# Optimization experiments

Measured on AMD Instinct MI355X. Metric: run time of the kernel, lower is better.

The kernel has to match this reference:

```python
import jax, jax.numpy as jnp
import numpy as np

HID, NHEAD, NLAYERS = 128, 8, 6
BS, H, W = 1, 64, 128
HD = HID // NHEAD  # head dim = 16


def layer_norm(x, g, b, eps=1e-5):
    m = jnp.mean(x, -1, keepdims=True)
    v = jnp.mean((x - m) ** 2, -1, keepdims=True)
    return (x - m) * jax.lax.rsqrt(v + eps) * g + b


def mha_relative(query, kv, in_w, in_b, out_w, out_b, pos_enc, pos_idx, attn_mask, is_self):
    # query/kv: [W, N, C]; in_w: [3C, C]; pos_enc: [2W-1, C]; pos_idx: [W*W]
    w, n, c = query.shape
    if is_self:
        q, k, v = jnp.split(query @ in_w.T + in_b, 3, axis=-1)
    else:
        q = query @ in_w[:c].T + in_b[:c]
        k, v = jnp.split(kv @ in_w[c:].T + in_b[c:], 2, axis=-1)
    # relative positional bias: gather [2W-1,C] -> [W,W,C], project with q/k weights
    pos_sel = pos_enc[pos_idx].reshape(w, w, c)
    q_r, k_r = jnp.split(pos_sel @ in_w[:2 * c].T + in_b[:2 * c], 2, axis=-1)
    scale = HD ** -0.5
    q = (q * scale).reshape(w, n, NHEAD, HD)
    k = k.reshape(w, n, NHEAD, HD)
    v = v.reshape(w, n, NHEAD, HD)
    q_r = (q_r * scale).reshape(w, w, NHEAD, HD)
    k_r = k_r.reshape(w, w, NHEAD, HD)
    attn = (jnp.einsum('wnec,vnec->newv', q, k)
            + jnp.einsum('wnec,wvec->newv', q, k_r)
            + jnp.einsum('vnec,wvec->newv', k, q_r))  # [N,E,W,W]
    if attn_mask is not None:
        attn = attn + attn_mask[None, None]
    raw_attn = attn.sum(axis=1)  # [N,W,W] head-summed raw scores
    a = jax.nn.softmax(attn, axis=-1)
    v_o = jnp.einsum('newv,vnec->wnec', a, v).reshape(w, n, c)
    return v_o @ out_w.T + out_b, raw_attn


def setup_inputs() -> dict:
    key = jax.random.key(0)
    ks = jax.random.split(key, 8)
    f32 = jnp.float32
    s = 0.02
    d = {}
    d['feat_left'] = jax.random.normal(ks[0], (BS, HID, H, W), f32)
    d['feat_right'] = jax.random.normal(ks[1], (BS, HID, H, W), f32)
    d['pos_enc'] = jax.random.normal(ks[2], (2 * W - 1, HID), f32)
    d['self_ln_g'] = jnp.ones((NLAYERS, HID), f32)
    d['self_ln_b'] = jnp.zeros((NLAYERS, HID), f32)
    d['self_in_w'] = jax.random.normal(ks[3], (NLAYERS, 3 * HID, HID), f32) * s
    d['self_in_b'] = jnp.zeros((NLAYERS, 3 * HID), f32)
    d['self_out_w'] = jax.random.normal(ks[4], (NLAYERS, HID, HID), f32) * s
    d['self_out_b'] = jnp.zeros((NLAYERS, HID), f32)
    d['cross_ln1_g'] = jnp.ones((NLAYERS, HID), f32)
    d['cross_ln1_b'] = jnp.zeros((NLAYERS, HID), f32)
    d['cross_ln2_g'] = jnp.ones((NLAYERS, HID), f32)
    d['cross_ln2_b'] = jnp.zeros((NLAYERS, HID), f32)
    d['cross_in_w'] = jax.random.normal(ks[5], (NLAYERS, 3 * HID, HID), f32) * s
    d['cross_in_b'] = jnp.zeros((NLAYERS, 3 * HID), f32)
    d['cross_out_w'] = jax.random.normal(ks[6], (NLAYERS, HID, HID), f32) * s
    d['cross_out_b'] = jnp.zeros((NLAYERS, HID), f32)
    return d


def reference(feat_left, feat_right, pos_enc, self_ln_g, self_ln_b, self_in_w, self_in_b,
              self_out_w, self_out_b, cross_ln1_g, cross_ln1_b, cross_ln2_g, cross_ln2_b,
              cross_in_w, cross_in_b, cross_out_w, cross_out_b):
    bs, c, hn, w = feat_left.shape  # bs must be 1 (as in source)
    # [N,C,H,W] -> [W, H*N, C]
    fl = jnp.transpose(feat_left, (3, 2, 0, 1)).reshape(w, hn * bs, c)
    fr = jnp.transpose(feat_right, (3, 2, 0, 1)).reshape(w, hn * bs, c)
    HN = hn * bs
    # pos_indexes[i,j] = (w-1-i) + j, values in [0, 2w-2]
    pos_idx = ((w - 1 - jnp.arange(w))[:, None] + jnp.arange(w)[None, :]).reshape(-1)
    causal = jnp.triu(jnp.full((w, w), -jnp.inf, feat_left.dtype), k=1)
    feat = jnp.concatenate([fl, fr], axis=1)  # [W, 2HN, C]
    raw_attn = None
    for i in range(NLAYERS):
        # self attention over concatenated left+right rows
        f2 = layer_norm(feat, self_ln_g[i], self_ln_b[i])
        upd, _ = mha_relative(f2, f2, self_in_w[i], self_in_b[i], self_out_w[i],
                              self_out_b[i], pos_enc, pos_idx, None, True)
        feat = feat + upd
        left, right = feat[:, :HN], feat[:, HN:]
        # cross attention: left queries attend to norm2(right)
        # (source computes a right-update with norm1/flipped pos but discards it)
        l2 = layer_norm(left, cross_ln1_g[i], cross_ln1_b[i])
        r2 = layer_norm(right, cross_ln2_g[i], cross_ln2_b[i])
        mask = causal if i == NLAYERS - 1 else None
        upd, raw_attn = mha_relative(l2, r2, cross_in_w[i], cross_in_b[i], cross_out_w[i],
                                     cross_out_b[i], pos_enc, pos_idx, mask, False)
        left = left + upd
        feat = jnp.concatenate([left, right], axis=1)
    # [HN,W,W] -> [bs, hn, W, W]
    return jnp.transpose(raw_attn.reshape(hn, bs, w, w), (1, 0, 2, 3))
```

## Files before the change

kernel.cpp:

```cpp
#include <hip/hip_runtime.h>
#include <cmath>

#define CDIM 128

typedef __attribute__((ext_vector_type(8))) short bf16x8;
typedef __attribute__((ext_vector_type(4))) float f32x4;
typedef unsigned short u16;

__device__ inline unsigned pk2(float a, float b) {
    unsigned ua = __float_as_uint(a) + 0x8000u;
    unsigned ub = __float_as_uint(b) + 0x8000u;
    return (ua >> 16) | (ub & 0xffff0000u);
}
__device__ inline u16 pk1(float x) {
    return (u16)((__float_as_uint(x) + 0x8000u) >> 16);
}
__device__ inline float ubf(u16 u) { return __uint_as_float(((unsigned)u) << 16); }
__device__ inline float ulo(unsigned u) { return __uint_as_float(u << 16); }
__device__ inline float uhi(unsigned u) { return __uint_as_float(u & 0xffff0000u); }

__global__ __launch_bounds__(256) void setup1_kernel(const float* __restrict__ w0,
                                                     const float* __restrict__ w1,
                                                     const float* __restrict__ w2,
                                                     const float* __restrict__ w3,
                                                     const float* __restrict__ b0,
                                                     const float* __restrict__ b1,
                                                     u16* __restrict__ wout,
                                                     float* __restrict__ bout,
                                                     const float* __restrict__ FL,
                                                     const float* __restrict__ FR,
                                                     u16* __restrict__ feat) {
    __shared__ float t[32][33];
    int bb = blockIdx.x;
    if (bb < 786) {
        int idx = bb * 256 + threadIdx.x;
        if (idx < 196608) {
            const float* src; long off4; u16* dst;
            if (idx < 73728)       { src = w0; off4 = idx;           dst = wout; }
            else if (idx < 147456) { src = w1; off4 = idx - 73728;   dst = wout + 294912; }
            else if (idx < 172032) { src = w2; off4 = idx - 147456;  dst = wout + 589824; }
            else                   { src = w3; off4 = idx - 172032;  dst = wout + 688128; }
            float4 f = *(const float4*)(src + off4 * 4);
            *(uint2*)(dst + off4 * 4) = make_uint2(pk2(f.x, f.y), pk2(f.z, f.w));
        } else {
            int tt = idx - 196608;
            if (tt < 4608) bout[tt] = (tt < 2304) ? b0[tt] : b1[tt - 2304];
        }
        return;
    }
    int b = bb - 786;
    int cb = b & 3, wb = (b >> 2) & 3, n = b >> 4;
    const float* src = (n < 64) ? FL : FR;
    int nn = n & 63;
    int j = threadIdx.x & 31, i0 = threadIdx.x >> 5;
    #pragma unroll
    for (int p = 0; p < 4; p++) {
        int i = i0 + p * 8;
        t[i][j] = src[(cb * 32 + i) * 8192 + nn * 128 + wb * 32 + j];
    }
    __syncthreads();
    #pragma unroll
    for (int p = 0; p < 4; p++) {
        int i = i0 + p * 8;
        feat[((long)(wb * 32 + i) * 128 + n) * 128 + cb * 32 + j] = pk1(t[j][i]);
    }
}

__global__ __launch_bounds__(256, 4) void setup2_kernel(const u16* __restrict__ feat,
                                                        const float* __restrict__ g,
                                                        const float* __restrict__ b,
                                                        u16* __restrict__ lnB,
                                                        const float* __restrict__ Apos,
                                                        const u16* __restrict__ Wpp,
                                                        const float* __restrict__ biaspp,
                                                        u16* __restrict__ Cpp,
                                                        float scale) {
    __shared__ __align__(16) u16 sA[64 * 136];
    __shared__ __align__(16) u16 sW[64 * 136];
    int bb = blockIdx.x;
    int tid = threadIdx.x;
    if (bb < 1024) {
        int wv = tid >> 6, lane = tid & 63;
        float g0 = g[lane * 2], b0 = b[lane * 2];
        float g1 = g[lane * 2 + 1], b1 = b[lane * 2 + 1];
        #pragma unroll
        for (int rr = 0; rr < 4; rr++) {
            long m = (long)bb * 16 + wv * 4 + rr;
            unsigned u = *(const unsigned*)(feat + m * 128 + lane * 2);
            float x0 = ulo(u), x1 = uhi(u);
            float s = x0 + x1, q = x0 * x0 + x1 * x1;
            #pragma unroll
            for (int off = 1; off < 64; off <<= 1) {
                s += __shfl_xor(s, off);
                q += __shfl_xor(q, off);
            }
            float mean = s * (1.f / 128.f);
            float var = q * (1.f / 128.f) - mean * mean;
            float rs = rsqrtf(var + 1e-5f);
            float y0 = (x0 - mean) * rs * g0 + b0;
            float y1 = (x1 - mean) * rs * g1 + b1;
            *(unsigned*)(lnB + m * 128 + lane * 2) = pk2(y0, y1);
        }
        return;
    }
    int b2 = bb - 1024;
    int bx = b2 & 3, byy = (b2 >> 2) & 3, z = b2 >> 4;
    const int M = 255, N = 256;
    const u16* W = Wpp + (long)z * 49152;
    const float* bias = biaspp + z * 384;
    u16* C = Cpp + (long)z * 65280;
    int row0 = byy * 64, col0 = bx * 64;
    float4 zf4 = make_float4(0.f, 0.f, 0.f, 0.f);
    int kc = tid & 31;
    #pragma unroll
    for (int i = 0; i < 8; i++) {
        int r = (tid + i * 256) >> 5;
        int m = row0 + r;
        int jn = col0 + r;
        float4 fa = (m < M) ? *(const float4*)(Apos + (long)m * 128 + kc * 4) : zf4;
        uint2 uw = make_uint2(0u, 0u);
        if (jn < N) uw = *(const uint2*)(W + (long)jn * 128 + kc * 4);
        *(uint2*)&sA[r * 136 + kc * 4] = make_uint2(pk2(fa.x, fa.y), pk2(fa.z, fa.w));
        *(uint2*)&sW[r * 136 + kc * 4] = uw;
    }
    __syncthreads();

    int wv = tid >> 6, lane = tid & 63, quad = lane >> 4, col = lane & 15;
    f32x4 z4 = {0.f, 0.f, 0.f, 0.f};
    f32x4 acc0 = z4, acc1 = z4, acc2 = z4, acc3 = z4;
    #pragma unroll
    for (int kb = 0; kb < 4; kb++) {
        bf16x8 a = *(const bf16x8*)&sA[(wv * 16 + col) * 136 + kb * 32 + quad * 8];
        bf16x8 b0 = *(const bf16x8*)&sW[(0 * 16 + col) * 136 + kb * 32 + quad * 8];
        bf16x8 b1 = *(const bf16x8*)&sW[(1 * 16 + col) * 136 + kb * 32 + quad * 8];
        bf16x8 b2 = *(const bf16x8*)&sW[(2 * 16 + col) * 136 + kb * 32 + quad * 8];
        bf16x8 b3 = *(const bf16x8*)&sW[(3 * 16 + col) * 136 + kb * 32 + quad * 8];
        acc0 = __builtin_amdgcn_mfma_f32_16x16x32_bf16(a, b0, acc0, 0, 0, 0);
        acc1 = __builtin_amdgcn_mfma_f32_16x16x32_bf16(a, b1, acc1, 0, 0, 0);
        acc2 = __builtin_amdgcn_mfma_f32_16x16x32_bf16(a, b2, acc2, 0, 0, 0);
        acc3 = __builtin_amdgcn_mfma_f32_16x16x32_bf16(a, b3, acc3, 0, 0, 0);
    }
    int mrow = row0 + wv * 16 + quad * 4;
    #pragma unroll
    for (int tc = 0; tc < 4; tc++) {
        f32x4 acc = tc == 0 ? acc0 : tc == 1 ? acc1 : tc == 2 ? acc2 : acc3;
        int jn = col0 + tc * 16 + col;
        if (jn >= N) continue;
        float bs = bias[jn];
        float sc = (jn < 128) ? scale : 1.f;
        long db = ((long)(jn >> 4) * 255) * 16 + (jn & 15);
        #pragma unroll
        for (int reg = 0; reg < 4; reg++) {
            int m = mrow + reg;
            if (m >= M) continue;
            C[db + (long)m * 16] = pk1((acc[reg] + bs) * sc);
        }
    }
}

__global__ __launch_bounds__(256, 3) void gemm_qkv128_kernel(const u16* __restrict__ A,
                                                             const u16* __restrict__ W,
                                                             const float* __restrict__ bias,
                                                             u16* __restrict__ C,
                                                             float scale) {
    __shared__ __align__(16) u16 sA[128 * 136];
    __shared__ __align__(16) u16 sW[64 * 136];
    int tid = threadIdx.x;
    int row0 = blockIdx.y * 128, col0 = blockIdx.x * 64;
    int kc = tid & 31;
    #pragma unroll
    for (int i = 0; i < 16; i++) {
        int r = (tid + i * 256) >> 5;
        *(uint2*)&sA[r * 136 + kc * 4] =
            *(const uint2*)(A + (long)(row0 + r) * 128 + kc * 4);
    }
    #pragma unroll
    for (int i = 0; i < 8; i++) {
        int r = (tid + i * 256) >> 5;
        *(uint2*)&sW[r * 136 + kc * 4] =
            *(const uint2*)(W + (long)(col0 + r) * 128 + kc * 4);
    }
    __syncthreads();

    int wv = tid >> 6, lane = tid & 63, quad = lane >> 4, col = lane & 15;
    f32x4 z4 = {0.f, 0.f, 0.f, 0.f};
    f32x4 accA0 = z4, accA1 = z4, accA2 = z4, accA3 = z4;
    f32x4 accB0 = z4, accB1 = z4, accB2 = z4, accB3 = z4;
    #pragma unroll
    for (int kb = 0; kb < 4; kb++) {
        bf16x8 a0 = *(const bf16x8*)&sA[(wv * 32 + col) * 136 + kb * 32 + quad * 8];
        bf16x8 a1 = *(const bf16x8*)&sA[(wv * 32 + 16 + col) * 136 + kb * 32 + quad * 8];
        bf16x8 b0 = *(const bf16x8*)&sW[(0 * 16 + col) * 136 + kb * 32 + quad * 8];
        bf16x8 b1 = *(const bf16x8*)&sW[(1 * 16 + col) * 136 + kb * 32 + quad * 8];
        bf16x8 b2 = *(const bf16x8*)&sW[(2 * 16 + col) * 136 + kb * 32 + quad * 8];
        bf16x8 b3 = *(const bf16x8*)&sW[(3 * 16 + col) * 136 + kb * 32 + quad * 8];
        accA0 = __builtin_amdgcn_mfma_f32_16x16x32_bf16(a0, b0, accA0, 0, 0, 0);
        accA1 = __builtin_amdgcn_mfma_f32_16x16x32_bf16(a0, b1, accA1, 0, 0, 0);
        accA2 = __builtin_amdgcn_mfma_f32_16x16x32_bf16(a0, b2, accA2, 0, 0, 0);
        accA3 = __builtin_amdgcn_mfma_f32_16x16x32_bf16(a0, b3, accA3, 0, 0, 0);
        accB0 = __builtin_amdgcn_mfma_f32_16x16x32_bf16(a1, b0, accB0, 0, 0, 0);
        accB1 = __builtin_amdgcn_mfma_f32_16x16x32_bf16(a1, b1, accB1, 0, 0, 0);
        accB2 = __builtin_amdgcn_mfma_f32_16x16x32_bf16(a1, b2, accB2, 0, 0, 0);
        accB3 = __builtin_amdgcn_mfma_f32_16x16x32_bf16(a1, b3, accB3, 0, 0, 0);
    }
    long woff = (long)blockIdx.y * 16;
    #pragma unroll
    for (int st = 0; st < 2; st++) {
        int nrow = wv * 32 + st * 16 + quad * 4;
        #pragma unroll
        for (int tc = 0; tc < 4; tc++) {
            f32x4 acc;
            if (st == 0) acc = tc == 0 ? accA0 : tc == 1 ? accA1 : tc == 2 ? accA2 : accA3;
            else         acc = tc == 0 ? accB0 : tc == 1 ? accB1 : tc == 2 ? accB2 : accB3;
            int jn = col0 + tc * 16 + col;
            float bs = bias[jn];
            float sc = (jn < 128) ? scale : 1.f;
            long db = ((long)(jn >> 4) * 128) * 2048 + woff + (jn & 15);
            #pragma unroll
            for (int reg = 0; reg < 4; reg++)
                C[db + (long)(nrow + reg) * 2048] = pk1((acc[reg] + bs) * sc);
        }
    }
}

__global__ __launch_bounds__(256, 2) void f1_out_self_cqkv_kernel(
        const u16* __restrict__ A,
        const u16* __restrict__ W,
        const float* __restrict__ bias,
        u16* __restrict__ feat,
        const float* __restrict__ g1, const float* __restrict__ b1,
        const float* __restrict__ g2, const float* __restrict__ b2,
        const float* __restrict__ sng, const float* __restrict__ snb,
        u16* __restrict__ lnB,
        const u16* __restrict__ Wcr,
        const float* __restrict__ biac,
        u16* __restrict__ QKV,
        float scale) {
    __shared__ __align__(16) u16 sA[64 * 136];
    __shared__ __align__(16) u16 sW[128 * 136];
    int tid = threadIdx.x;
    int by = blockIdx.x;
    int row0 = by * 64;
    int right = by & 1;
    int w = by >> 1;
    int kc = tid & 31;
    uint2 pw[16];
    #pragma unroll
    for (int i = 0; i < 8; i++) {
        int r = (tid + i * 256) >> 5;
        *(uint2*)&sA[r * 136 + kc * 4] = *(const uint2*)(A + (long)(row0 + r) * 128 + kc * 4);
    }
    #pragma unroll
    for (int i = 0; i < 16; i++) {
        int r = (tid + i * 256) >> 5;
        *(uint2*)&sW[r * 136 + kc * 4] = *(const uint2*)(W + (long)r * 128 + kc * 4);
    }
    {
        int w0 = right ? 128 : 0;
        #pragma unroll
        for (int i = 0; i < 16; i++) {
            int r = (tid + i * 256) >> 5;
            pw[i] = *(const uint2*)(Wcr + (long)(w0 + r) * 128 + kc * 4);
        }
    }
    __syncthreads();

    int wv = tid >> 6, lane = tid & 63, quad = lane >> 4, col = lane & 15;
    f32x4 acc[8] = {};
    #pragma unroll
    for (int kb = 0; kb < 4; kb++) {
        bf16x8 a = *(const bf16x8*)&sA[(wv * 16 + col) * 136 + kb * 32 + quad * 8];
        #pragma unroll
        for (int tc = 0; tc < 8; tc++) {
            bf16x8 b = *(const bf16x8*)&sW[(tc * 16 + col) * 136 + kb * 32 + quad * 8];
            acc[tc] = __builtin_amdgcn_mfma_f32_16x16x32_bf16(a, b, acc[tc], 0, 0, 0);
        }
    }
    __syncthreads();

    #pragma unroll
    for (int i = 0; i < 16; i++) {
        int r = (tid + i * 256) >> 5;
        *(uint2*)&sW[r * 136 + kc * 4] = pw[i];
    }
    if (right) {
        #pragma unroll
        for (int i = 0; i < 16; i++) {
            int r = (tid + i * 256) >> 5;
            pw[i] = *(const uint2*)(Wcr + (long)(256 + r) * 128 + kc * 4);
        }
    }

    const float* gA = right ? g2 : g1;
    const float* bA = right ? b2 : b1;
    float gAv[8], bAv[8], gBv[8], bBv[8], bsv[8];
    bool doB = (sng != nullptr) && right;
    #pragma unroll
    for (int tc = 0; tc < 8; tc++) {
        int jn = tc * 16 + col;
        gAv[tc] = gA[jn]; bAv[tc] = bA[jn]; bsv[tc] = bias[jn];
        if (doB) { gBv[tc] = sng[jn]; bBv[tc] = snb[jn]; }
    }
    #pragma unroll
    for (int reg = 0; reg < 4; reg++) {
        int nloc = wv * 16 + quad * 4 + reg;
        long m = row0 + nloc;
        long rb = m * 128;
        float o[8];
        float s = 0.f, q = 0.f;
        #pragma unroll
        for (int tc = 0; tc < 8; tc++) {
            int jn = tc * 16 + col;
            float v = acc[tc][reg] + bsv[tc] + ubf(feat[rb + jn]);
            o[tc] = v; s += v; q += v * v;
        }
        #pragma unroll
        for (int off = 1; off < 16; off <<= 1) {
            s += __shfl_xor(s, off);
            q += __shfl_xor(q, off);
        }
        float mean = s * (1.f / 128.f);
        float var = q * (1.f / 128.f) - mean * mean;
        float rs = rsqrtf(var + 1e-5f);
        #pragma unroll
        for (int tc = 0; tc < 8; tc++) {
            int jn = tc * 16 + col;
            feat[rb + jn] = pk1(o[tc]);
            float ln = (o[tc] - mean) * rs;
            sA[nloc * 136 + jn] = pk1(ln * gAv[tc] + bAv[tc]);
            if (doB) lnB[rb + jn] = pk1(ln * gBv[tc] + bBv[tc]);
        }
    }
    __syncthreads();

    int passes = right ? 2 : 1;
    #pragma unroll
    for (int p = 0; p < 2; p++) {
        if (p >= passes) break;
        if (p) {
            __syncthreads();
            #pragma unroll
            for (int i = 0; i < 16; i++) {
                int r = (tid + i * 256) >> 5;
                *(uint2*)&sW[r * 136 + kc * 4] = pw[i];
            }
            __syncthreads();
        }
        int wrow0 = right ? (128 + p * 128) : 0;
        f32x4 acb[8] = {};
        #pragma unroll
        for (int kb = 0; kb < 4; kb++) {
            bf16x8 a = *(const bf16x8*)&sA[(wv * 16 + col) * 136 + kb * 32 + quad * 8];
            #pragma unroll
            for (int tc = 0; tc < 8; tc++) {
                bf16x8 b = *(const bf16x8*)&sW[(tc * 16 + col) * 136 + kb * 32 + quad * 8];
                acb[tc] = __builtin_amdgcn_mfma_f32_16x16x32_bf16(a, b, acb[tc], 0, 0, 0);
            }
        }
        float sc = right ? 1.f : scale;
        int nrow = wv * 16 + quad * 4;
        #pragma unroll
        for (int tc = 0; tc < 8; tc++) {
            int jn = tc * 16 + col;
            float bs = biac[wrow0 + jn];
            int strip = right ? (8 + p * 8 + (jn >> 4)) : (jn >> 4);
            long db = (long)strip * 131072 + w * 16 + (jn & 15);
            #pragma unroll
            for (int reg = 0; reg < 4; reg++)
                QKV[db + (long)(nrow + reg) * 2048] = pk1((acb[tc][reg] + bs) * sc);
        }
    }
}

__global__ __launch_bounds__(256, 2) void f2_out_cross_qkv_kernel(
        const u16* __restrict__ A,
        const u16* __restrict__ W,
        const float* __restrict__ bias,
        u16* __restrict__ feat,
        const float* __restrict__ sng,
        const float* __restrict__ snb,
        const u16* __restrict__ lnBg,
        const u16* __restrict__ Wsl,
        const float* __restrict__ biasq,
        u16* __restrict__ QKV,
        float scale) {
    __shared__ __align__(16) u16 sA[64 * 136];
    __shared__ __align__(16) u16 sW[128 * 136];
    int tid = threadIdx.x;
    int t = blockIdx.x;
    int right = t & 1, w = t >> 1;
    int kc = tid & 31;
    uint2 pw[16];
    if (!right) {
        #pragma unroll
        for (int i = 0; i < 8; i++) {
            int r = (tid + i * 256) >> 5;
            *(uint2*)&sA[r * 136 + kc * 4] =
                *(const uint2*)(A + (long)(w * 64 + r) * 128 + kc * 4);
        }
        #pragma unroll
        for (int i = 0; i < 16; i++) {
            int r = (tid + i * 256) >> 5;
            *(uint2*)&sW[r * 136 + kc * 4] = *(const uint2*)(W + (long)r * 128 + kc * 4);
        }
    } else {
        #pragma unroll
        for (int i = 0; i < 8; i++) {
            int r = (tid + i * 256) >> 5;
            *(uint2*)&sA[r * 136 + kc * 4] =
                *(const uint2*)(lnBg + (long)(w * 128 + 64 + r) * 128 + kc * 4);
        }
    }
    #pragma unroll
    for (int i = 0; i < 16; i++) {
        int r = (tid + i * 256) >> 5;
        pw[i] = *(const uint2*)(Wsl + (long)r * 128 + kc * 4);
    }
    __syncthreads();

    int wv = tid >> 6, lane = tid & 63, quad = lane >> 4, col = lane & 15;
    if (!right) {
        f32x4 acc[8] = {};
        #pragma unroll
        for (int kb = 0; kb < 4; kb++) {
            bf16x8 a = *(const bf16x8*)&sA[(wv * 16 + col) * 136 + kb * 32 + quad * 8];
            #pragma unroll
            for (int tc = 0; tc < 8; tc++) {
                bf16x8 b = *(const bf16x8*)&sW[(tc * 16 + col) * 136 + kb * 32 + quad * 8];
                acc[tc] = __builtin_amdgcn_mfma_f32_16x16x32_bf16(a, b, acc[tc], 0, 0, 0);
            }
        }
        __syncthreads();
        float gBv[8], bBv[8], bsv[8];
        #pragma unroll
        for (int tc = 0; tc < 8; tc++) {
            int jn = tc * 16 + col;
            gBv[tc] = sng[jn]; bBv[tc] = snb[jn]; bsv[tc] = bias[jn];
        }
        #pragma unroll
        for (int reg = 0; reg < 4; reg++) {
            int nloc = wv * 16 + quad * 4 + reg;
            long rb = ((long)w * 128 + nloc) * 128;
            float o[8];
            float s = 0.f, q = 0.f;
            #pragma unroll
            for (int tc = 0; tc < 8; tc++) {
                int jn = tc * 16 + col;
                float v = acc[tc][reg] + bsv[tc] + ubf(feat[rb + jn]);
                o[tc] = v; s += v; q += v * v;
            }
            #pragma unroll
            for (int off = 1; off < 16; off <<= 1) {
                s += __shfl_xor(s, off);
                q += __shfl_xor(q, off);
            }
            float mean = s * (1.f / 128.f);
            float var = q * (1.f / 128.f) - mean * mean;
            float rs = rsqrtf(var + 1e-5f);
            #pragma unroll
            for (int tc = 0; tc < 8; tc++) {
                int jn = tc * 16 + col;
                feat[rb + jn] = pk1(o[tc]);
                sA[nloc * 136 + jn] = pk1((o[tc] - mean) * rs * gBv[tc] + bBv[tc]);
            }
        }
    }
    #pragma unroll
    for (int i = 0; i < 16; i++) {
        int r = (tid + i * 256) >> 5;
        *(uint2*)&sW[r * 136 + kc * 4] = pw[i];
    }
    #pragma unroll
    for (int i = 0; i < 16; i++) {
        int r = (tid + i * 256) >> 5;
        pw[i] = *(const uint2*)(Wsl + (long)(128 + r) * 128 + kc * 4);
    }
    __syncthreads();

    int n0 = right ? 64 : 0;
    #pragma unroll
    for (int p = 0; p < 3; p++) {
        if (p) {
            __syncthreads();
            #pragma unroll
            for (int i = 0; i < 16; i++) {
                int r = (tid + i * 256) >> 5;
                *(uint2*)&sW[r * 136 + kc * 4] = pw[i];
            }
            if (p < 2) {
                #pragma unroll
                for (int i = 0; i < 16; i++) {
                    int r = (tid + i * 256) >> 5;
                    pw[i] = *(const uint2*)(Wsl + (long)(256 + r) * 128 + kc * 4);
                }
            }
            __syncthreads();
        }
        f32x4 ac[8] = {};
        #pragma unroll
        for (int kb = 0; kb < 4; kb++) {
            bf16x8 a = *(const bf16x8*)&sA[(wv * 16 + col) * 136 + kb * 32 + quad * 8];
            #pragma unroll
            for (int tc = 0; tc < 8; tc++) {
                bf16x8 b = *(const bf16x8*)&sW[(tc * 16 + col) * 136 + kb * 32 + quad * 8];
                ac[tc] = __builtin_amdgcn_mfma_f32_16x16x32_bf16(a, b, ac[tc], 0, 0, 0);
            }
        }
        int nrow = n0 + wv * 16 + quad * 4;
        #pragma unroll
        for (int tc = 0; tc < 8; tc++) {
            int jn = p * 128 + tc * 16 + col;
            float bs = biasq[jn];
            float sc = (jn < 128) ? scale : 1.f;
            long db = (long)(jn >> 4) * 262144 + w * 16 + (jn & 15);
            #pragma unroll
            for (int reg = 0; reg < 4; reg++)
                QKV[db + (long)(nrow + reg) * 2048] = pk1((ac[tc][reg] + bs) * sc);
        }
    }
}

__global__ __launch_bounds__(512, 8) void attn_kernel(const u16* __restrict__ QKV,
                                                      const u16* __restrict__ PPL,
                                                      u16* __restrict__ VO,
                                                      float* __restrict__ RAW,
                                                      int NN, int causal) {
    __shared__ __align__(16) u16 sm[19584];
    const int SKV = 0, SA = 2176;
    int e = blockIdx.x, n = blockIdx.y;
    int tid = threadIdx.x;
    int wv = tid >> 6, lane = tid & 63, quad = lane >> 4, col = lane & 15;

    const u16* qb = QKV + ((long)e * NN + n) * 2048;
    const u16* kb = QKV + ((long)(8 + e) * NN + n) * 2048;
    const u16* vb = QKV + ((long)(16 + e) * NN + n) * 2048;
    const u16* qr = PPL + (long)e * 4080;
    const u16* kr = PPL + (long)(8 + e) * 4080;

    bf16x8 zf = {0, 0, 0, 0, 0, 0, 0, 0};
    f32x4 z4 = {0.f, 0.f, 0.f, 0.f};
    bf16x8 aQ = zf, aK = zf;
    if (quad < 2) {
        aQ = *(const bf16x8*)(qb + (wv * 16 + col) * 16 + quad * 8);
        aK = *(const bf16x8*)(kb + (wv * 16 + col) * 16 + quad * 8);
    }
    {
        int row = tid >> 2, c = tid & 3;
        *(uint2*)&sm[SKV + row * 16 + c * 4] = *(const uint2*)(kb + row * 16 + c * 4);
    }
    __syncthreads();

    f32x4 s1[8];
    #pragma unroll
    for (int tv = 0; tv < 8; tv++) {
        bf16x8 b = zf;
        if (quad < 2) b = *(const bf16x8*)&sm[SKV + (tv * 16 + col) * 16 + quad * 8];
        s1[tv] = __builtin_amdgcn_mfma_f32_16x16x32_bf16(aQ, b, z4, 0, 0, 0);
    }
    int wbq = wv * 16 + quad * 4;
    int s2lo = 7 - wv;
    #pragma unroll 3
    for (int tt = 0; tt < 9; tt++) {
        int tr = s2lo + tt;
        bf16x8 b = zf;
        if (quad < 2) b = *(const bf16x8*)(kr + (tr * 16 + col) * 16 + quad * 8);
        f32x4 d = __builtin_amdgcn_mfma_f32_16x16x32_bf16(aQ, b, z4, 0, 0, 0);
        #pragma unroll
        for (int reg = 0; reg < 4; reg++) {
            int v = tr * 16 + col - 127 + wbq + reg;
            if (v >= 0 && v < 128) sm[SA + (wbq + reg) * 136 + v] = pk1(d[reg]);
        }
    }
    __syncthreads();
    {
        int row = tid >> 2, c = tid & 3;
        uint2 uv = *(const uint2*)(vb + row * 16 + c * 4);
        sm[SKV + (c * 4 + 0) * 136 + row] = (u16)(uv.x & 0xffffu);
        sm[SKV + (c * 4 + 1) * 136 + row] = (u16)(uv.x >> 16);
        sm[SKV + (c * 4 + 2) * 136 + row] = (u16)(uv.y & 0xffffu);
        sm[SKV + (c * 4 + 3) * 136 + row] = (u16)(uv.y >> 16);
    }
    #pragma unroll 3
    for (int tt = 0; tt < 9; tt++) {
        int tr = wv + tt;
        bf16x8 b = zf;
        if (quad < 2) b = *(const bf16x8*)(qr + (tr * 16 + col) * 16 + quad * 8);
        f32x4 d = __builtin_amdgcn_mfma_f32_16x16x32_bf16(aK, b, z4, 0, 0, 0);
        #pragma unroll
        for (int reg = 0; reg < 4; reg++) {
            int v = wbq + reg;
            int w = 127 + v - (tr * 16 + col);
            if (w >= 0 && w < 128) {
                int addr = SA + w * 136 + v;
                sm[addr] = pk1(ubf(sm[addr]) + d[reg]);
            }
        }
    }
    __syncthreads();

    float rs0 = 0.f, rs1 = 0.f, rs2 = 0.f, rs3 = 0.f;
    #pragma unroll
    for (int tv = 0; tv < 8; tv++) {
        f32x4 c = s1[tv];
        int v = tv * 16 + col;
        #pragma unroll
        for (int reg = 0; reg < 4; reg++) {
            int w = wbq + reg;
            int addr = SA + w * 136 + v;
            float a = c[reg] + ubf(sm[addr]);
            bool live = !(causal && v > w);
            float p = live ? __expf(a) : 0.f;
            if (RAW) RAW[(long)n * 16384 + w * 128 + v] = live ? a : 0.f;
            sm[addr] = pk1(p);
            if (reg == 0) rs0 += p; else if (reg == 1) rs1 += p;
            else if (reg == 2) rs2 += p; else rs3 += p;
        }
    }
    #pragma unroll
    for (int o = 1; o < 16; o <<= 1) {
        rs0 += __shfl_xor(rs0, o);
        rs1 += __shfl_xor(rs1, o);
        rs2 += __shfl_xor(rs2, o);
        rs3 += __shfl_xor(rs3, o);
    }
    __syncthreads();

    f32x4 o4 = z4;
    #pragma unroll
    for (int kb = 0; kb < 4; kb++) {
        bf16x8 a = *(const bf16x8*)&sm[SA + (wv * 16 + col) * 136 + kb * 32 + quad * 8];
        bf16x8 b = *(const bf16x8*)&sm[SKV + col * 136 + kb * 32 + quad * 8];
        o4 = __builtin_amdgcn_mfma_f32_16x16x32_bf16(a, b, o4, 0, 0, 0);
    }
    float iv0 = 1.f / rs0, iv1 = 1.f / rs1, iv2 = 1.f / rs2, iv3 = 1.f / rs3;
    VO[(long)((wbq + 0) * NN + n) * CDIM + e * 16 + col] = pk1(o4[0] * iv0);
    VO[(long)((wbq + 1) * NN + n) * CDIM + e * 16 + col] = pk1(o4[1] * iv1);
    VO[(long)((wbq + 2) * NN + n) * CDIM + e * 16 + col] = pk1(o4[2] * iv2);
    VO[(long)((wbq + 3) * NN + n) * CDIM + e * 16 + col] = pk1(o4[3] * iv3);
}

extern "C" void kernel_launch(void* const* d_in, const int* in_sizes, int n_in,
                              void* d_out, int out_size, void* d_ws, size_t ws_size,
                              hipStream_t stream) {
    const float* FL         = (const float*)d_in[0];
    const float* FR         = (const float*)d_in[1];
    const float* pos_enc    = (const float*)d_in[2];
    const float* self_ln_g  = (const float*)d_in[3];
    const float* self_ln_b  = (const float*)d_in[4];
    const float* self_in_w  = (const float*)d_in[5];
    const float* self_in_b  = (const float*)d_in[6];
    const float* self_out_w = (const float*)d_in[7];
    const float* self_out_b = (const float*)d_in[8];
    const float* cr_ln1_g   = (const float*)d_in[9];
    const float* cr_ln1_b   = (const float*)d_in[10];
    const float* cr_ln2_g   = (const float*)d_in[11];
    const float* cr_ln2_b   = (const float*)d_in[12];
    const float* cr_in_w    = (const float*)d_in[13];
    const float* cr_in_b    = (const float*)d_in[14];
    const float* cr_out_w   = (const float*)d_in[15];
    const float* cr_out_b   = (const float*)d_in[16];

    float* ws       = (float*)d_ws;
    u16*   feat     = (u16*)ws;
    u16*   vo       = (u16*)(ws + 1048576);
    u16*   qkvS     = (u16*)(ws + 2097152);
    u16*   pp_self  = (u16*)(ws + 5242880);
    u16*   pp_cross = pp_self + 391680;
    u16*   wbf      = (u16*)(ws + 5634560);
    u16*   wsel_in  = wbf;
    u16*   wcr_in   = wbf + 294912;
    u16*   wsel_out = wbf + 589824;
    u16*   wcr_out  = wbf + 688128;
    float* bin      = ws + 6027776;
    u16*   lnB      = (u16*)(ws + 7080960);
    float* out      = (float*)d_out;

    const float scale = 0.25f;

    setup1_kernel<<<2834, 256, 0, stream>>>(self_in_w, cr_in_w, self_out_w, cr_out_w,
                                            self_in_b, cr_in_b, wbf, bin,
                                            FL, FR, feat);
    setup2_kernel<<<1216, 256, 0, stream>>>(feat, self_ln_g, self_ln_b, lnB,
                                            pos_enc, wsel_in, bin, pp_self, scale);
    gemm_qkv128_kernel<<<dim3(6, 128), 256, 0, stream>>>(lnB, wsel_in,
                                                         self_in_b, qkvS, scale);

    for (int i = 0; i < 6; i++) {
        int last = (i == 5);
        attn_kernel<<<dim3(8, 128), 512, 0, stream>>>(qkvS, pp_self + i * 65280,
                                                      vo, nullptr, 128, 0);
        f1_out_self_cqkv_kernel<<<256, 256, 0, stream>>>(vo, wsel_out + i * 16384,
                                                         self_out_b + i * 128, feat,
                                                         cr_ln1_g + i * 128, cr_ln1_b + i * 128,
                                                         cr_ln2_g + i * 128, cr_ln2_b + i * 128,
                                                         last ? nullptr : self_ln_g + (i + 1) * 128,
                                                         last ? nullptr : self_ln_b + (i + 1) * 128,
                                                         lnB,
                                                         wcr_in + i * 49152,
                                                         cr_in_b + i * 384,
                                                         qkvS, scale);

        attn_kernel<<<dim3(8, 64), 512, 0, stream>>>(qkvS, pp_cross + i * 65280,
                                                     vo, last ? out : nullptr,
                                                     64, last);
        if (!last) {
            f2_out_cross_qkv_kernel<<<256, 256, 0, stream>>>(vo, wcr_out + i * 16384,
                                                             cr_out_b + i * 128, feat,
                                                             self_ln_g + (i + 1) * 128,
                                                             self_ln_b + (i + 1) * 128,
                                                             lnB,
                                                             wsel_in + (i + 1) * 49152,
                                                             self_in_b + (i + 1) * 384,
                                                             qkvS, scale);
        }
    }
}
```

Measured before the change: 480.9 us.

## Warp-specialize fused out-proj/QKV kernels with 512 threads and weight prefetch

```diff
diff --git a/kernel.cpp b/kernel.cpp
--- a/kernel.cpp
+++ b/kernel.cpp
@@ -223,7 +223,7 @@
     }
 }
 
-__global__ __launch_bounds__(256, 2) void f1_out_self_cqkv_kernel(
+__global__ __launch_bounds__(512, 1) void f1_out_self_cqkv_kernel(
         const u16* __restrict__ A,
         const u16* __restrict__ W,
         const float* __restrict__ bias,
@@ -243,136 +243,168 @@
     int row0 = by * 64;
     int right = by & 1;
     int w = by >> 1;
-    int kc = tid & 31;
-    uint2 pw[16];
-    #pragma unroll
-    for (int i = 0; i < 8; i++) {
-        int r = (tid + i * 256) >> 5;
-        *(uint2*)&sA[r * 136 + kc * 4] = *(const uint2*)(A + (long)(row0 + r) * 128 + kc * 4);
-    }
-    #pragma unroll
-    for (int i = 0; i < 16; i++) {
-        int r = (tid + i * 256) >> 5;
-        *(uint2*)&sW[r * 136 + kc * 4] = *(const uint2*)(W + (long)r * 128 + kc * 4);
-    }
-    {
+    int wv = tid >> 6, lane = tid & 63, quad = lane >> 4, col = lane & 15;
+    int koff = quad * 8;
+    int t2 = tid & 255;
+    int kc = t2 & 31;
+    uint2 pw0[16], pw1[16];
+
+    if (tid < 256) {
+        #pragma unroll
+        for (int i = 0; i < 8; i++) {
+            int r = (t2 + i * 256) >> 5;
+            *(uint2*)&sA[r * 136 + kc * 4] = *(const uint2*)(A + (long)(row0 + r) * 128 + kc * 4);
+        }
+        #pragma unroll
+        for (int i = 0; i < 16; i++) {
+            int r = (t2 + i * 256) >> 5;
+            *(uint2*)&sW[r * 136 + kc * 4] = *(const uint2*)(W + (long)r * 128 + kc * 4);
+        }
+    } else {
         int w0 = right ? 128 : 0;
         #pragma unroll
         for (int i = 0; i < 16; i++) {
-            int r = (tid + i * 256) >> 5;
-            pw[i] = *(const uint2*)(Wcr + (long)(w0 + r) * 128 + kc * 4);
-        }
-    }
-    __syncthreads();
-
-    int wv = tid >> 6, lane = tid & 63, quad = lane >> 4, col = lane & 15;
+            int r = (t2 + i * 256) >> 5;
+            pw0[i] = *(const uint2*)(Wcr + (long)(w0 + r) * 128 + kc * 4);
+        }
+        if (right) {
+            #pragma unroll
+            for (int i = 0; i < 16; i++) {
+                int r = (t2 + i * 256) >> 5;
+                pw1[i] = *(const uint2*)(Wcr + (long)(256 + r) * 128 + kc * 4);
+            }
+        }
+    }
+    __syncthreads();
+
     f32x4 acc[8] = {};
-    #pragma unroll
-    for (int kb = 0; kb < 4; kb++) {
-        bf16x8 a = *(const bf16x8*)&sA[(wv * 16 + col) * 136 + kb * 32 + quad * 8];
-        #pragma unroll
-        for (int tc = 0; tc < 8; tc++) {
-            bf16x8 b = *(const bf16x8*)&sW[(tc * 16 + col) * 136 + kb * 32 + quad * 8];
-            acc[tc] = __builtin_amdgcn_mfma_f32_16x16x32_bf16(a, b, acc[tc], 0, 0, 0);
-        }
-    }
-    __syncthreads();
-
-    #pragma unroll
-    for (int i = 0; i < 16; i++) {
-        int r = (tid + i * 256) >> 5;
-        *(uint2*)&sW[r * 136 + kc * 4] = pw[i];
-    }
-    if (right) {
-        #pragma unroll
-        for (int i = 0; i < 16; i++) {
-            int r = (tid + i * 256) >> 5;
-            pw[i] = *(const uint2*)(Wcr + (long)(256 + r) * 128 + kc * 4);
-        }
-    }
-
-    const float* gA = right ? g2 : g1;
-    const float* bA = right ? b2 : b1;
-    float gAv[8], bAv[8], gBv[8], bBv[8], bsv[8];
-    bool doB = (sng != nullptr) && right;
-    #pragma unroll
-    for (int tc = 0; tc < 8; tc++) {
-        int jn = tc * 16 + col;
-        gAv[tc] = gA[jn]; bAv[tc] = bA[jn]; bsv[tc] = bias[jn];
-        if (doB) { gBv[tc] = sng[jn]; bBv[tc] = snb[jn]; }
-    }
-    #pragma unroll
-    for (int reg = 0; reg < 4; reg++) {
-        int nloc = wv * 16 + quad * 4 + reg;
-        long m = row0 + nloc;
-        long rb = m * 128;
-        float o[8];
-        float s = 0.f, q = 0.f;
+    if (tid < 256) {
+        #pragma unroll
+        for (int kb = 0; kb < 4; kb++) {
+            bf16x8 a = *(const bf16x8*)&sA[(wv * 16 + col) * 136 + kb * 32 + koff];
+            #pragma unroll
+            for (int tc = 0; tc < 8; tc++) {
+                bf16x8 b = *(const bf16x8*)&sW[(tc * 16 + col) * 136 + kb * 32 + koff];
+                acc[tc] = __builtin_amdgcn_mfma_f32_16x16x32_bf16(a, b, acc[tc], 0, 0, 0);
+            }
+        }
+    }
+    __syncthreads();
+
+    if (tid < 256) {
+        const float* gA = right ? g2 : g1;
+        const float* bA = right ? b2 : b1;
+        float gAv[8], bAv[8], gBv[8], bBv[8], bsv[8];
+        bool doB = (sng != nullptr) && right;
         #pragma unroll
         for (int tc = 0; tc < 8; tc++) {
             int jn = tc * 16 + col;
-            float v = acc[tc][reg] + bsv[tc] + ubf(feat[rb + jn]);
-            o[tc] = v; s += v; q += v * v;
-        }
-        #pragma unroll
-        for (int off = 1; off < 16; off <<= 1) {
-            s += __shfl_xor(s, off);
-            q += __shfl_xor(q, off);
-        }
-        float mean = s * (1.f / 128.f);
-        float var = q * (1.f / 128.f) - mean * mean;
-        float rs = rsqrtf(var + 1e-5f);
-        #pragma unroll
-        for (int tc = 0; tc < 8; tc++) {
-            int jn = tc * 16 + col;
-            feat[rb + jn] = pk1(o[tc]);
-            float ln = (o[tc] - mean) * rs;
-            sA[nloc * 136 + jn] = pk1(ln * gAv[tc] + bAv[tc]);
-            if (doB) lnB[rb + jn] = pk1(ln * gBv[tc] + bBv[tc]);
-        }
-    }
-    __syncthreads();
-
-    int passes = right ? 2 : 1;
-    #pragma unroll
-    for (int p = 0; p < 2; p++) {
-        if (p >= passes) break;
-        if (p) {
-            __syncthreads();
-            #pragma unroll
-            for (int i = 0; i < 16; i++) {
-                int r = (tid + i * 256) >> 5;
-                *(uint2*)&sW[r * 136 + kc * 4] = pw[i];
-            }
-            __syncthreads();
-        }
-        int wrow0 = right ? (128 + p * 128) : 0;
-        f32x4 acb[8] = {};
+            gAv[tc] = gA[jn]; bAv[tc] = bA[jn]; bsv[tc] = bias[jn];
+            if (doB) { gBv[tc] = sng[jn]; bBv[tc] = snb[jn]; }
+        }
+        #pragma unroll
+        for (int reg = 0; reg < 4; reg++) {
+            int nloc = wv * 16 + quad * 4 + reg;
+            long m = row0 + nloc;
+            long rb = m * 128;
+            float o[8];
+            float s = 0.f, q = 0.f;
+            #pragma unroll
+            for (int tc = 0; tc < 8; tc++) {
+                int jn = tc * 16 + col;
+                float v = acc[tc][reg] + bsv[tc] + ubf(feat[rb + jn]);
+                o[tc] = v; s += v; q += v * v;
+            }
+            #pragma unroll
+            for (int off = 1; off < 16; off <<= 1) {
+                s += __shfl_xor(s, off);
+                q += __shfl_xor(q, off);
+            }
+            float mean = s * (1.f / 128.f);
+            float var = q * (1.f / 128.f) - mean * mean;
+            float rs = rsqrtf(var + 1e-5f);
+            #pragma unroll
+            for (int tc = 0; tc < 8; tc++) {
+                int jn = tc * 16 + col;
+                feat[rb + jn] = pk1(o[tc]);
+                float ln = (o[tc] - mean) * rs;
+                sA[nloc * 136 + jn] = pk1(ln * gAv[tc] + bAv[tc]);
+                if (doB) lnB[rb + jn] = pk1(ln * gBv[tc] + bBv[tc]);
+            }
+        }
+    } else {
+        #pragma unroll
+        for (int i = 0; i < 16; i++) {
+            int r = (t2 + i * 256) >> 5;
+            *(uint2*)&sW[r * 136 + kc * 4] = pw0[i];
+        }
+    }
+    __syncthreads();
+
+    int rowgrp = wv & 3, colgrp = wv >> 2;
+    bf16x8 pa[4];
+    #pragma unroll
+    for (int kb = 0; kb < 4; kb++)
+        pa[kb] = *(const bf16x8*)&sA[(rowgrp * 16 + col) * 136 + kb * 32 + koff];
+    float sc = right ? 1.f : scale;
+    int nrow = rowgrp * 16 + quad * 4;
+    {
+        int wrow0 = right ? 128 : 0;
+        f32x4 acb[4] = {};
         #pragma unroll
         for (int kb = 0; kb < 4; kb++) {
-            bf16x8 a = *(const bf16x8*)&sA[(wv * 16 + col) * 136 + kb * 32 + quad * 8];
-            #pragma unroll
-            for (int tc = 0; tc < 8; tc++) {
-                bf16x8 b = *(const bf16x8*)&sW[(tc * 16 + col) * 136 + kb * 32 + quad * 8];
-                acb[tc] = __builtin_amdgcn_mfma_f32_16x16x32_bf16(a, b, acb[tc], 0, 0, 0);
-            }
-        }
-        float sc = right ? 1.f : scale;
-        int nrow = wv * 16 + quad * 4;
-        #pragma unroll
-        for (int tc = 0; tc < 8; tc++) {
-            int jn = tc * 16 + col;
+            #pragma unroll
+            for (int tc = 0; tc < 4; tc++) {
+                int jn = colgrp * 64 + tc * 16 + col;
+                bf16x8 b = *(const bf16x8*)&sW[jn * 136 + kb * 32 + koff];
+                acb[tc] = __builtin_amdgcn_mfma_f32_16x16x32_bf16(pa[kb], b, acb[tc], 0, 0, 0);
+            }
+        }
+        #pragma unroll
+        for (int tc = 0; tc < 4; tc++) {
+            int jn = colgrp * 64 + tc * 16 + col;
             float bs = biac[wrow0 + jn];
-            int strip = right ? (8 + p * 8 + (jn >> 4)) : (jn >> 4);
+            int strip = right ? (8 + (jn >> 4)) : (jn >> 4);
             long db = (long)strip * 131072 + w * 16 + (jn & 15);
             #pragma unroll
             for (int reg = 0; reg < 4; reg++)
                 QKV[db + (long)(nrow + reg) * 2048] = pk1((acb[tc][reg] + bs) * sc);
         }
     }
+    if (right) {
+        __syncthreads();
+        if (tid >= 256) {
+            #pragma unroll
+            for (int i = 0; i < 16; i++) {
+                int r = (t2 + i * 256) >> 5;
+                *(uint2*)&sW[r * 136 + kc * 4] = pw1[i];
+            }
+        }
+        __syncthreads();
+        f32x4 acb[4] = {};
+        #pragma unroll
+        for (int kb = 0; kb < 4; kb++) {
+            #pragma unroll
+            for (int tc = 0; tc < 4; tc++) {
+                int jn = colgrp * 64 + tc * 16 + col;
+                bf16x8 b = *(const bf16x8*)&sW[jn * 136 + kb * 32 + koff];
+                acb[tc] = __builtin_amdgcn_mfma_f32_16x16x32_bf16(pa[kb], b, acb[tc], 0, 0, 0);
+            }
+        }
+        #pragma unroll
+        for (int tc = 0; tc < 4; tc++) {
+            int jn = colgrp * 64 + tc * 16 + col;
+            float bs = biac[256 + jn];
+            int strip = 16 + (jn >> 4);
+            long db = (long)strip * 131072 + w * 16 + (jn & 15);
+            #pragma unroll
+            for (int reg = 0; reg < 4; reg++)
+                QKV[db + (long)(nrow + reg) * 2048] = pk1((acb[tc][reg] + bs) * 1.f);
+        }
+    }
 }
 
-__global__ __launch_bounds__(256, 2) void f2_out_cross_qkv_kernel(
+__global__ __launch_bounds__(512, 1) void f2_out_cross_qkv_kernel(
         const u16* __restrict__ A,
         const u16* __restrict__ W,
         const float* __restrict__ bias,
@@ -389,133 +421,196 @@
     int tid = threadIdx.x;
     int t = blockIdx.x;
     int right = t & 1, w = t >> 1;
-    int kc = tid & 31;
-    uint2 pw[16];
+    int wv = tid >> 6, lane = tid & 63, quad = lane >> 4, col = lane & 15;
+    int koff = quad * 8;
+    int t2 = tid & 255;
+    int kc = t2 & 31;
+    int rowgrp = wv & 3, colgrp = wv >> 2;
+    bf16x8 pa[4];
+
     if (!right) {
-        #pragma unroll
-        for (int i = 0; i < 8; i++) {
-            int r = (tid + i * 256) >> 5;
-            *(uint2*)&sA[r * 136 + kc * 4] =
-                *(const uint2*)(A + (long)(w * 64 + r) * 128 + kc * 4);
-        }
-        #pragma unroll
-        for (int i = 0; i < 16; i++) {
-            int r = (tid + i * 256) >> 5;
-            *(uint2*)&sW[r * 136 + kc * 4] = *(const uint2*)(W + (long)r * 128 + kc * 4);
-        }
-    } else {
-        #pragma unroll
-        for (int i = 0; i < 8; i++) {
-            int r = (tid + i * 256) >> 5;
-            *(uint2*)&sA[r * 136 + kc * 4] =
-                *(const uint2*)(lnBg + (long)(w * 128 + 64 + r) * 128 + kc * 4);
-        }
-    }
-    #pragma unroll
-    for (int i = 0; i < 16; i++) {
-        int r = (tid + i * 256) >> 5;
-        pw[i] = *(const uint2*)(Wsl + (long)r * 128 + kc * 4);
-    }
-    __syncthreads();
-
-    int wv = tid >> 6, lane = tid & 63, quad = lane >> 4, col = lane & 15;
-    if (!right) {
+        uint2 pw0[16], pw1[16];
+        if (tid < 256) {
+            #pragma unroll
+            for (int i = 0; i < 8; i++) {
+                int r = (t2 + i * 256) >> 5;
+                *(uint2*)&sA[r * 136 + kc * 4] =
+                    *(const uint2*)(A + (long)(w * 64 + r) * 128 + kc * 4);
+            }
+            #pragma unroll
+            for (int i = 0; i < 16; i++) {
+                int r = (t2 + i * 256) >> 5;
+                *(uint2*)&sW[r * 136 + kc * 4] = *(const uint2*)(W + (long)r * 128 + kc * 4);
+            }
+        } else {
+            #pragma unroll
+            for (int i = 0; i < 16; i++) {
+                int r = (t2 + i * 256) >> 5;
+                pw0[i] = *(const uint2*)(Wsl + (long)r * 128 + kc * 4);
+            }
+            #pragma unroll
+            for (int i = 0; i < 16; i++) {
+                int r = (t2 + i * 256) >> 5;
+                pw1[i] = *(const uint2*)(Wsl + (long)(128 + r) * 128 + kc * 4);
+            }
+        }
+        __syncthreads();
+
         f32x4 acc[8] = {};
-        #pragma unroll
-        for (int kb = 0; kb < 4; kb++) {
-            bf16x8 a = *(const bf16x8*)&sA[(wv * 16 + col) * 136 + kb * 32 + quad * 8];
-            #pragma unroll
-            for (int tc = 0; tc < 8; tc++) {
-                bf16x8 b = *(const bf16x8*)&sW[(tc * 16 + col) * 136 + kb * 32 + quad * 8];
-                acc[tc] = __builtin_amdgcn_mfma_f32_16x16x32_bf16(a, b, acc[tc], 0, 0, 0);
+        if (tid < 256) {
+            #pragma unroll
+            for (int kb = 0; kb < 4; kb++) {
+                bf16x8 a = *(const bf16x8*)&sA[(wv * 16 + col) * 136 + kb * 32 + koff];
+                #pragma unroll
+                for (int tc = 0; tc < 8; tc++) {
+                    bf16x8 b = *(const bf16x8*)&sW[(tc * 16 + col) * 136 + kb * 32 + koff];
+                    acc[tc] = __builtin_amdgcn_mfma_f32_16x16x32_bf16(a, b, acc[tc], 0, 0, 0);
+                }
             }
         }
         __syncthreads();
-        float gBv[8], bBv[8], bsv[8];
-        #pragma unroll
-        for (int tc = 0; tc < 8; tc++) {
-            int jn = tc * 16 + col;
-            gBv[tc] = sng[jn]; bBv[tc] = snb[jn]; bsv[tc] = bias[jn];
-        }
-        #pragma unroll
-        for (int reg = 0; reg < 4; reg++) {
-            int nloc = wv * 16 + quad * 4 + reg;
-            long rb = ((long)w * 128 + nloc) * 128;
-            float o[8];
-            float s = 0.f, q = 0.f;
+
+        if (tid < 256) {
+            float gBv[8], bBv[8], bsv[8];
             #pragma unroll
             for (int tc = 0; tc < 8; tc++) {
                 int jn = tc * 16 + col;
-                float v = acc[tc][reg] + bsv[tc] + ubf(feat[rb + jn]);
-                o[tc] = v; s += v; q += v * v;
-            }
-            #pragma unroll
-            for (int off = 1; off < 16; off <<= 1) {
-                s += __shfl_xor(s, off);
-                q += __shfl_xor(q, off);
-            }
-            float mean = s * (1.f / 128.f);
-            float var = q * (1.f / 128.f) - mean * mean;
-            float rs = rsqrtf(var + 1e-5f);
-            #pragma unroll
-            for (int tc = 0; tc < 8; tc++) {
-                int jn = tc * 16 + col;
-                feat[rb + jn] = pk1(o[tc]);
-                sA[nloc * 136 + jn] = pk1((o[tc] - mean) * rs * gBv[tc] + bBv[tc]);
-            }
-        }
-    }
-    #pragma unroll
-    for (int i = 0; i < 16; i++) {
-        int r = (tid + i * 256) >> 5;
-        *(uint2*)&sW[r * 136 + kc * 4] = pw[i];
-    }
-    #pragma unroll
-    for (int i = 0; i < 16; i++) {
-        int r = (tid + i * 256) >> 5;
-        pw[i] = *(const uint2*)(Wsl + (long)(128 + r) * 128 + kc * 4);
-    }
-    __syncthreads();
-
-    int n0 = right ? 64 : 0;
-    #pragma unroll
-    for (int p = 0; p < 3; p++) {
-        if (p) {
-            __syncthreads();
+                gBv[tc] = sng[jn]; bBv[tc] = snb[jn]; bsv[tc] = bias[jn];
+            }
+            #pragma unroll
+            for (int reg = 0; reg < 4; reg++) {
+                int nloc = wv * 16 + quad * 4 + reg;
+                long rb = ((long)w * 128 + nloc) * 128;
+                float o[8];
+                float s = 0.f, q = 0.f;
+                #pragma unroll
+                for (int tc = 0; tc < 8; tc++) {
+                    int jn = tc * 16 + col;
+                    float v = acc[tc][reg] + bsv[tc] + ubf(feat[rb + jn]);
+                    o[tc] = v; s += v; q += v * v;
+                }
+                #pragma unroll
+                for (int off = 1; off < 16; off <<= 1) {
+                    s += __shfl_xor(s, off);
+                    q += __shfl_xor(q, off);
+                }
+                float mean = s * (1.f / 128.f);
+                float var = q * (1.f / 128.f) - mean * mean;
+                float rs = rsqrtf(var + 1e-5f);
+                #pragma unroll
+                for (int tc = 0; tc < 8; tc++) {
+                    int jn = tc * 16 + col;
+                    feat[rb + jn] = pk1(o[tc]);
+                    sA[nloc * 136 + jn] = pk1((o[tc] - mean) * rs * gBv[tc] + bBv[tc]);
+                }
+            }
+        } else {
             #pragma unroll
             for (int i = 0; i < 16; i++) {
-                int r = (tid + i * 256) >> 5;
-                *(uint2*)&sW[r * 136 + kc * 4] = pw[i];
-            }
-            if (p < 2) {
+                int r = (t2 + i * 256) >> 5;
+                *(uint2*)&sW[r * 136 + kc * 4] = pw0[i];
+            }
+            #pragma unroll
+            for (int i = 0; i < 16; i++) {
+                int r = (t2 + i * 256) >> 5;
+                pw0[i] = *(const uint2*)(Wsl + (long)(256 + r) * 128 + kc * 4);
+            }
+        }
+        __syncthreads();
+
+        #pragma unroll
+        for (int kb = 0; kb < 4; kb++)
+            pa[kb] = *(const bf16x8*)&sA[(rowgrp * 16 + col) * 136 + kb * 32 + koff];
+
+        int nrow0 = rowgrp * 16 + quad * 4;
+        #pragma unroll
+        for (int p = 0; p < 3; p++) {
+            if (p) {
+                __syncthreads();
+                if (tid >= 256) {
+                    #pragma unroll
+                    for (int i = 0; i < 16; i++) {
+                        int r = (t2 + i * 256) >> 5;
+                        *(uint2*)&sW[r * 136 + kc * 4] = (p == 1) ? pw1[i] : pw0[i];
+                    }
+                }
+                __syncthreads();
+            }
+            f32x4 ac[4] = {};
+            #pragma unroll
+            for (int kb = 0; kb < 4; kb++) {
                 #pragma unroll
-                for (int i = 0; i < 16; i++) {
-                    int r = (tid + i * 256) >> 5;
-                    pw[i] = *(const uint2*)(Wsl + (long)(256 + r) * 128 + kc * 4);
+                for (int tc = 0; tc < 4; tc++) {
+                    int jc = colgrp * 64 + tc * 16 + col;
+                    bf16x8 b = *(const bf16x8*)&sW[jc * 136 + kb * 32 + koff];
+                    ac[tc] = __builtin_amdgcn_mfma_f32_16x16x32_bf16(pa[kb], b, ac[tc], 0, 0, 0);
                 }
             }
-            __syncthreads();
-        }
-        f32x4 ac[8] = {};
-        #pragma unroll
-        for (int kb = 0; kb < 4; kb++) {
-            bf16x8 a = *(const bf16x8*)&sA[(wv * 16 + col) * 136 + kb * 32 + quad * 8];
-            #pragma unroll
-            for (int tc = 0; tc < 8; tc++) {
-                bf16x8 b = *(const bf16x8*)&sW[(tc * 16 + col) * 136 + kb * 32 + quad * 8];
-                ac[tc] = __builtin_amdgcn_mfma_f32_16x16x32_bf16(a, b, ac[tc], 0, 0, 0);
-            }
-        }
-        int nrow = n0 + wv * 16 + quad * 4;
-        #pragma unroll
-        for (int tc = 0; tc < 8; tc++) {
-            int jn = p * 128 + tc * 16 + col;
-            float bs = biasq[jn];
-            float sc = (jn < 128) ? scale : 1.f;
-            long db = (long)(jn >> 4) * 262144 + w * 16 + (jn & 15);
-            #pragma unroll
-            for (int reg = 0; reg < 4; reg++)
-                QKV[db + (long)(nrow + reg) * 2048] = pk1((ac[tc][reg] + bs) * sc);
+            #pragma unroll
+            for (int tc = 0; tc < 4; tc++) {
+                int jn = p * 128 + colgrp * 64 + tc * 16 + col;
+                float bs = biasq[jn];
+                float sc = (jn < 128) ? scale : 1.f;
+                long db = (long)(jn >> 4) * 262144 + w * 16 + (jn & 15);
+                #pragma unroll
+                for (int reg = 0; reg < 4; reg++)
+                    QKV[db + (long)(nrow0 + reg) * 2048] = pk1((ac[tc][reg] + bs) * sc);
+            }
+        }
+    } else {
+        uint2 pwr[16];
+        #pragma unroll
+        for (int i = 0; i < 8; i++) {
+            int r = (tid >> 5) + i * 16;
+            *(uint2*)&sW[r * 136 + (tid & 31) * 4] =
+                *(const uint2*)(Wsl + (long)r * 128 + (tid & 31) * 4);
+        }
+        int wbase = (tid < 256) ? 256 : 128;
+        #pragma unroll
+        for (int i = 0; i < 16; i++) {
+            int r = (t2 + i * 256) >> 5;
+            pwr[i] = *(const uint2*)(Wsl + (long)(wbase + r) * 128 + kc * 4);
+        }
+        #pragma unroll
+        for (int kb = 0; kb < 4; kb++)
+            pa[kb] = *(const bf16x8*)(lnBg + (long)(w * 128 + 64 + rowgrp * 16 + col) * 128 + kb * 32 + koff);
+        __syncthreads();
+
+        int nrow0 = 64 + rowgrp * 16 + quad * 4;
+        #pragma unroll
+        for (int p = 0; p < 3; p++) {
+            if (p) {
+                __syncthreads();
+                bool mine = (p == 1) ? (tid >= 256) : (tid < 256);
+                if (mine) {
+                    #pragma unroll
+                    for (int i = 0; i < 16; i++) {
+                        int r = (t2 + i * 256) >> 5;
+                        *(uint2*)&sW[r * 136 + kc * 4] = pwr[i];
+                    }
+                }
+                __syncthreads();
+            }
+            f32x4 ac[4] = {};
+            #pragma unroll
+            for (int kb = 0; kb < 4; kb++) {
+                #pragma unroll
+                for (int tc = 0; tc < 4; tc++) {
+                    int jc = colgrp * 64 + tc * 16 + col;
+                    bf16x8 b = *(const bf16x8*)&sW[jc * 136 + kb * 32 + koff];
+                    ac[tc] = __builtin_amdgcn_mfma_f32_16x16x32_bf16(pa[kb], b, ac[tc], 0, 0, 0);
+                }
+            }
+            #pragma unroll
+            for (int tc = 0; tc < 4; tc++) {
+                int jn = p * 128 + colgrp * 64 + tc * 16 + col;
+                float bs = biasq[jn];
+                float sc = (jn < 128) ? scale : 1.f;
+                long db = (long)(jn >> 4) * 262144 + w * 16 + (jn & 15);
+                #pragma unroll
+                for (int reg = 0; reg < 4; reg++)
+                    QKV[db + (long)(nrow0 + reg) * 2048] = pk1((ac[tc][reg] + bs) * sc);
+            }
         }
     }
 }
@@ -689,7 +784,7 @@
         int last = (i == 5);
         attn_kernel<<<dim3(8, 128), 512, 0, stream>>>(qkvS, pp_self + i * 65280,
                                                       vo, nullptr, 128, 0);
-        f1_out_self_cqkv_kernel<<<256, 256, 0, stream>>>(vo, wsel_out + i * 16384,
+        f1_out_self_cqkv_kernel<<<256, 512, 0, stream>>>(vo, wsel_out + i * 16384,
                                                          self_out_b + i * 128, feat,
                                                          cr_ln1_g + i * 128, cr_ln1_b + i * 128,
                                                          cr_ln2_g + i * 128, cr_ln2_b + i * 128,
@@ -704,7 +799,7 @@
                                                      vo, last ? out : nullptr,
                                                      64, last);
         if (!last) {
-            f2_out_cross_qkv_kernel<<<256, 256, 0, stream>>>(vo, wcr_out + i * 16384,
+            f2_out_cross_qkv_kernel<<<256, 512, 0, stream>>>(vo, wcr_out + i * 16384,
                                                              cr_out_b + i * 128, feat,
                                                              self_ln_g + (i + 1) * 128,
                                                              self_ln_b + (i + 1) * 128,
```

New measurement: 449.8 us. 6.5% less time.
